# Performance work log

Hardware: AMD Instinct MI355X
Metric: run time of the kernel (lower is better)

Reference implementation:

```python
import jax, jax.numpy as jnp
import numpy as np

B = 8
A = 1614
TOPN = 6
IOU_THR = 0.25
PAD = 224
OUT = 224

def _make_anchors():
    # 6 anchor shapes on the 14x14 map, 6 on 7x7, 9 on 4x4 -> 1614 total,
    # ordered anchor-type-major then row-major spatial to match the [C,H,W] flatten
    # of the tidy conv outputs (as generate_default_anchor_maps does in NTS-Net).
    specs = [
        (14, 32.0, [(48, 48), (64, 48), (48, 64), (80, 80), (96, 64), (64, 96)]),
        (7, 64.0, [(96, 96), (128, 96), (96, 128), (160, 160), (192, 128), (128, 192)]),
        (4, 112.0, [(192, 192), (256, 192), (192, 256), (288, 288), (320, 256), (256, 320), (352, 352), (384, 320), (320, 384)]),
    ]
    blocks = []
    for fm, stride, sizes in specs:
        c = (np.arange(fm) + 0.5) * stride
        cy, cx = np.meshgrid(c, c, indexing='ij')
        for (h, w) in sizes:
            blocks.append(np.stack([cy - h / 2, cx - w / 2, cy + h / 2, cx + w / 2], -1).reshape(-1, 4))
    a = (np.concatenate(blocks, 0) + PAD).astype(np.int64)  # mimic (edge_anchors+224).astype(int)
    return a.astype(np.float32)  # [1614,4] (y0,x0,y1,x1) in padded-image coords

def _conv(x, w, b, stride, pad):
    y = jax.lax.conv_general_dilated(x, w, (stride, stride), [(pad, pad), (pad, pad)],
                                     dimension_numbers=('NCHW', 'OIHW', 'NCHW'))
    return y + b[None, :, None, None]

def _rpn_scores(rpn, wd1, bd1, wd2, bd2, wd3, bd3, wt1, bt1, wt2, bt2, wt3, bt3):
    b = rpn.shape[0]
    d1 = jax.nn.relu(_conv(rpn, wd1, bd1, 1, 1))   # [B,128,14,14]
    d2 = jax.nn.relu(_conv(d1, wd2, bd2, 2, 1))    # [B,128,7,7]
    d3 = jax.nn.relu(_conv(d2, wd3, bd3, 2, 1))    # [B,128,4,4]
    t1 = _conv(d1, wt1, bt1, 1, 0).reshape(b, -1)  # [B,1176]
    t2 = _conv(d2, wt2, bt2, 1, 0).reshape(b, -1)  # [B,294]
    t3 = _conv(d3, wt3, bt3, 1, 0).reshape(b, -1)  # [B,144]
    return jnp.concatenate([t1, t2, t3], axis=1)   # [B,1614]

def _nms_keep(boxes, scores):
    # Greedy NMS over all A anchors; returns keep mask in ORIGINAL anchor order.
    order = jnp.argsort(-scores)
    b = boxes[order]
    y0, x0, y1, x1 = b[:, 0], b[:, 1], b[:, 2], b[:, 3]
    area = (y1 - y0) * (x1 - x0)
    ih = jnp.clip(jnp.minimum(y1[:, None], y1[None, :]) - jnp.maximum(y0[:, None], y0[None, :]), 0)
    iw = jnp.clip(jnp.minimum(x1[:, None], x1[None, :]) - jnp.maximum(x0[:, None], x0[None, :]), 0)
    inter = ih * iw
    iou = inter / (area[:, None] + area[None, :] - inter)
    idx = jnp.arange(A)
    def body(i, supp):
        row = (iou[i] > IOU_THR) & (idx > i)
        return jnp.where(supp[i], supp, supp | row)
    supp = jax.lax.fori_loop(0, A, body, jnp.zeros((A,), bool))
    return jnp.zeros((A,), bool).at[order].set(~supp)

def _crop_resize(img, box):
    # img [3,Hp,Wp]; box int32 (x0,y0,x1,y1).
    # Equivalent to F.interpolate(img[:, y0:y1, x0:x1], (224,224), 'bilinear', align_corners=True)
    x0, y0, x1, y1 = box[0], box[1], box[2], box[3]
    t = jnp.arange(OUT, dtype=jnp.float32) / (OUT - 1)
    sy = y0.astype(jnp.float32) + t * (y1 - 1 - y0).astype(jnp.float32)
    sx = x0.astype(jnp.float32) + t * (x1 - 1 - x0).astype(jnp.float32)
    y0i = jnp.floor(sy).astype(jnp.int32); x0i = jnp.floor(sx).astype(jnp.int32)
    y1i = jnp.minimum(y0i + 1, y1 - 1);    x1i = jnp.minimum(x0i + 1, x1 - 1)
    wy = (sy - y0i.astype(jnp.float32))[None, :, None]
    wx = (sx - x0i.astype(jnp.float32))[None, None, :]
    g = lambda yi, xi: img[:, yi][:, :, xi]  # gather rows then cols -> [3,224,224]
    top = (1 - wx) * g(y0i, x0i) + wx * g(y0i, x1i)
    bot = (1 - wx) * g(y1i, x0i) + wx * g(y1i, x1i)
    return (1 - wy) * top + wy * bot

def setup_inputs():
    key = jax.random.key(0)
    ks = jax.random.split(key, 16)
    n = jax.random.normal
    return {
        'x': n(ks[0], (B, 3, 448, 448), jnp.float32),
        'rpn_feature': n(ks[1], (B, 2048, 14, 14), jnp.float32),
        'anchors': jnp.asarray(_make_anchors()),
        'wd1': 0.02 * n(ks[2], (128, 2048, 3, 3), jnp.float32), 'bd1': 0.01 * n(ks[3], (128,), jnp.float32),
        'wd2': 0.05 * n(ks[4], (128, 128, 3, 3), jnp.float32),  'bd2': 0.01 * n(ks[5], (128,), jnp.float32),
        'wd3': 0.05 * n(ks[6], (128, 128, 3, 3), jnp.float32),  'bd3': 0.01 * n(ks[7], (128,), jnp.float32),
        'wt1': 0.1 * n(ks[8], (6, 128, 1, 1), jnp.float32),     'bt1': 0.01 * n(ks[9], (6,), jnp.float32),
        'wt2': 0.1 * n(ks[10], (6, 128, 1, 1), jnp.float32),    'bt2': 0.01 * n(ks[11], (6,), jnp.float32),
        'wt3': 0.1 * n(ks[12], (9, 128, 1, 1), jnp.float32),    'bt3': 0.01 * n(ks[13], (9,), jnp.float32),
    }

def reference(x, rpn_feature, anchors, wd1, bd1, wd2, bd2, wd3, bd3, wt1, bt1, wt2, bt2, wt3, bt3):
    scores = _rpn_scores(rpn_feature, wd1, bd1, wd2, bd2, wd3, bd3, wt1, bt1, wt2, bt2, wt3, bt3)
    keep = jax.vmap(lambda s: _nms_keep(anchors, s))(scores)           # [B,A] bool
    masked = jnp.where(keep, scores, -jnp.inf)
    top_prob, top_idx = jax.lax.top_k(masked, TOPN)                    # [B,6]
    tb = anchors[top_idx]                                              # [B,6,4] (y0,x0,y1,x1)
    coords = jnp.stack([tb[..., 1], tb[..., 0], tb[..., 3], tb[..., 2]], -1)  # (x0,y0,x1,y1)
    x_pad = jnp.pad(x, ((0, 0), (0, 0), (PAD, PAD), (PAD, PAD)))       # [B,3,896,896]
    bint = coords.astype(jnp.int32)
    part_imgs = jax.vmap(lambda img, bs: jax.vmap(lambda bb: _crop_resize(img, bb))(bs))(x_pad, bint)  # [B,6,3,224,224]
    return part_imgs, coords, top_prob, top_idx
```

## Files before the change

### kernel.cpp

```cpp
#include <hip/hip_runtime.h>
#include <hip/hip_bf16.h>
#include <math.h>
#include <stdint.h>


#define OFF_COORDS 7225344
#define OFF_PROB   7225536
#define OFF_IDX    7225584
#define NA 1614
#define K1TOT 18432

typedef __attribute__((ext_vector_type(8)))  short  short8;
typedef __attribute__((ext_vector_type(16))) float  floatx16;

__device__ inline void split_bf16(float v, unsigned short& h, unsigned short& l)
{
    __hip_bfloat16 hb = __float2bfloat16(v);
    float hv = __bfloat162float(hb);
    __hip_bfloat16 lb = __float2bfloat16(v - hv);
    h = *reinterpret_cast<unsigned short*>(&hb);
    l = *reinterpret_cast<unsigned short*>(&lb);
}

__global__ __launch_bounds__(256) void k_prep(const float* __restrict__ rpn,
                                              const float* __restrict__ w1,
                                              const float* __restrict__ w2,
                                              const float* __restrict__ w3,
                                              unsigned short* __restrict__ ah,
                                              unsigned short* __restrict__ al,
                                              unsigned short* __restrict__ b1h,
                                              unsigned short* __restrict__ b1l,
                                              unsigned short* __restrict__ b2h,
                                              unsigned short* __restrict__ b2l,
                                              unsigned short* __restrict__ b3h,
                                              unsigned short* __restrict__ b3l)
{
    __shared__ float tileA[64][65];
    __shared__ float tileB[9][260];
    const int bid = blockIdx.x;
    const int t   = threadIdx.x;

    if (bid < 1024) {
        const int cib  = (bid & 31) * 64;
        const int posb = ((bid >> 5) & 3) * 64;
        const int b    = bid >> 7;
#pragma unroll
        for (int it = 0; it < 16; ++it) {
            int idx  = it * 256 + t;
            int cil  = idx >> 6;
            int posl = idx & 63;
            int pos  = posb + posl;
            int py = pos >> 4, px = pos & 15;
            int y = py - 1, x = px - 1;
            float v = 0.0f;
            if ((unsigned)y < 14u && (unsigned)x < 14u)
                v = rpn[((size_t)(b * 2048 + cib + cil) * 14 + y) * 14 + x];
            tileA[cil][posl] = v;
        }
        __syncthreads();
#pragma unroll
        for (int it = 0; it < 16; ++it) {
            int idx  = it * 256 + t;
            int posl = idx >> 6;
            int cil  = idx & 63;
            float v = tileA[cil][posl];
            unsigned short h, l;
            split_bf16(v, h, l);
            size_t o = (size_t)(b * 256 + posb + posl) * 2048 + cib + cil;
            ah[o] = h; al[o] = l;
        }
    } else if (bid < 2048) {
        const int lb  = bid - 1024;
        const int ci0 = (lb & 7) * 256;
        const int co  = lb >> 3;
        const float* wc = w1 + (size_t)co * K1TOT + (size_t)ci0 * 9;
#pragma unroll
        for (int it = 0; it < 9; ++it) {
            int i = it * 256 + t;
            float v = wc[i];
            tileB[i % 9][i / 9] = v;
        }
        __syncthreads();
#pragma unroll
        for (int tap = 0; tap < 9; ++tap) {
            float v = tileB[tap][t];
            unsigned short h, l;
            split_bf16(v, h, l);
            size_t o = (size_t)co * K1TOT + (size_t)tap * 2048 + ci0 + t;
            b1h[o] = h; b1l[o] = l;
        }
    } else {
        const int lb  = bid - 2048;
        const int tap = lb % 9;
        const int co  = lb / 9;
        const int z   = t >> 7;
        const int ci  = t & 127;
        const float* w = z ? w3 : w2;
        unsigned short* bh = z ? b3h : b2h;
        unsigned short* bl = z ? b3l : b2l;
        float v = w[((size_t)co * 128 + ci) * 9 + tap];
        unsigned short h, l;
        split_bf16(v, h, l);
        size_t o = (size_t)co * 1152 + tap * 128 + ci;
        bh[o] = h; bl[o] = l;
    }
}

template<int POSN, int OW, int STR, int CIN, int MTOT>
__global__ __launch_bounds__(256) void k_conv_mfma(const short* __restrict__ ah,
                                                   const short* __restrict__ al,
                                                   const short* __restrict__ bh,
                                                   const short* __restrict__ bl,
                                                   float* __restrict__ partial,
                                                   int chunk)
{
    constexpr int KTOT = CIN * 9;
    __shared__ short AsH[128][40];
    __shared__ short AsL[128][40];
    __shared__ short BsH[128][40];
    __shared__ short BsL[128][40];

    const int t     = threadIdx.x;
    const int lane  = t & 63;
    const int w     = t >> 6;
    const int wm    = (w & 1) * 64;
    const int wn    = (w >> 1) * 64;
    const int lm    = lane & 31;
    const int half  = lane >> 5;
    const int mbase = blockIdx.x * 128;
    const int k0    = blockIdx.y * chunk;
    const int k1    = (k0 + chunk < KTOT) ? (k0 + chunk) : KTOT;

    int arow[2], apos[2]; bool aval[2];
    const int akc = (t & 3) * 8;
#pragma unroll
    for (int i = 0; i < 2; ++i) {
        int row = ((i * 256 + t) >> 2);
        int m   = mbase + row;
        arow[i] = row;
        aval[i] = (m < MTOT);
        int mm = aval[i] ? m : 0;
        int b  = mm / POSN;
        int p  = mm - b * POSN;
        int y  = p / OW;
        int x  = p - y * OW;
        apos[i] = b * 256 + y * STR * 16 + x * STR;
    }

    floatx16 acc[2][2];
#pragma unroll
    for (int mf = 0; mf < 2; ++mf)
#pragma unroll
        for (int nf = 0; nf < 2; ++nf)
#pragma unroll
            for (int r = 0; r < 16; ++r) acc[mf][nf][r] = 0.0f;

    const short8 zero8 = {0, 0, 0, 0, 0, 0, 0, 0};

    for (int ks = k0; ks < k1; ks += 32) {
        const int tap = ks / CIN;
        const int ci0 = ks - tap * CIN;
        const int dy  = tap / 3, dx = tap - dy * 3;
#pragma unroll
        for (int i = 0; i < 2; ++i) {
            short8 vh = zero8, vl = zero8;
            if (aval[i]) {
                size_t g = (size_t)(apos[i] + dy * 16 + dx) * CIN + ci0 + akc;
                vh = *(const short8*)(ah + g);
                vl = *(const short8*)(al + g);
            }
            *(short8*)&AsH[arow[i]][akc] = vh;
            *(short8*)&AsL[arow[i]][akc] = vl;
        }
#pragma unroll
        for (int i = 0; i < 2; ++i) {
            int n = ((i * 256 + t) >> 2);
            size_t g = (size_t)n * KTOT + ks + akc;
            *(short8*)&BsH[n][akc] = *(const short8*)(bh + g);
            *(short8*)&BsL[n][akc] = *(const short8*)(bl + g);
        }
        __syncthreads();
#pragma unroll
        for (int kst = 0; kst < 2; ++kst) {
            const int koff = kst * 16 + half * 8;
            short8 a_h[2], a_l[2], b_h[2], b_l[2];
#pragma unroll
            for (int mf = 0; mf < 2; ++mf) {
                a_h[mf] = *(const short8*)&AsH[wm + mf * 32 + lm][koff];
                a_l[mf] = *(const short8*)&AsL[wm + mf * 32 + lm][koff];
            }
#pragma unroll
            for (int nf = 0; nf < 2; ++nf) {
                b_h[nf] = *(const short8*)&BsH[wn + nf * 32 + lm][koff];
                b_l[nf] = *(const short8*)&BsL[wn + nf * 32 + lm][koff];
            }
#pragma unroll
            for (int mf = 0; mf < 2; ++mf)
#pragma unroll
                for (int nf = 0; nf < 2; ++nf) {
                    acc[mf][nf] = __builtin_amdgcn_mfma_f32_32x32x16_bf16(
                        a_h[mf], b_h[nf], acc[mf][nf], 0, 0, 0);
                    acc[mf][nf] = __builtin_amdgcn_mfma_f32_32x32x16_bf16(
                        a_h[mf], b_l[nf], acc[mf][nf], 0, 0, 0);
                    acc[mf][nf] = __builtin_amdgcn_mfma_f32_32x32x16_bf16(
                        a_l[mf], b_h[nf], acc[mf][nf], 0, 0, 0);
                }
        }
        __syncthreads();
    }

    float* P = partial + (size_t)blockIdx.y * MTOT * 128;
#pragma unroll
    for (int mf = 0; mf < 2; ++mf)
#pragma unroll
        for (int nf = 0; nf < 2; ++nf)
#pragma unroll
            for (int r = 0; r < 16; ++r) {
                int row = (r & 3) + 8 * (r >> 2) + 4 * half;
                int m = mbase + wm + mf * 32 + row;
                int n = wn + nf * 32 + lm;
                if (m < MTOT) P[(size_t)m * 128 + n] = acc[mf][nf][r];
            }
}

template<int POSN, int OW, int STR, int CIN, int MTOT>
__global__ __launch_bounds__(128) void k_conv64(const short* __restrict__ ah,
                                                const short* __restrict__ al,
                                                const short* __restrict__ bh,
                                                const short* __restrict__ bl,
                                                float* __restrict__ partial,
                                                int chunk)
{
    constexpr int KTOT = CIN * 9;
    __shared__ short AsH[64][40];
    __shared__ short AsL[64][40];
    __shared__ short BsH[128][40];
    __shared__ short BsL[128][40];

    const int t     = threadIdx.x;
    const int lane  = t & 63;
    const int w     = t >> 6;
    const int wn    = w * 64;
    const int lm    = lane & 31;
    const int half  = lane >> 5;
    const int mbase = blockIdx.x * 64;
    const int kc    = blockIdx.y;
    const int k0    = kc * chunk;
    const int k1    = (k0 + chunk < KTOT) ? (k0 + chunk) : KTOT;

    const int akc = (t & 3) * 8;
    int arow[2], apos[2]; bool aval[2];
#pragma unroll
    for (int i = 0; i < 2; ++i) {
        int slot = i * 128 + t;
        int row  = slot >> 2;
        int m    = mbase + row;
        arow[i] = row;
        aval[i] = (m < MTOT);
        int mm = aval[i] ? m : 0;
        int b  = mm / POSN;
        int p  = mm - b * POSN;
        int y  = p / OW;
        int x  = p - y * OW;
        apos[i] = b * 256 + y * STR * 16 + x * STR;
    }

    floatx16 acc[2][2];
#pragma unroll
    for (int mf = 0; mf < 2; ++mf)
#pragma unroll
        for (int nf = 0; nf < 2; ++nf)
#pragma unroll
            for (int r = 0; r < 16; ++r) acc[mf][nf][r] = 0.0f;

    const short8 zero8 = {0, 0, 0, 0, 0, 0, 0, 0};

    for (int ks = k0; ks < k1; ks += 32) {
        const int tap = ks / CIN;
        const int ci0 = ks - tap * CIN;
        const int dy  = tap / 3, dx = tap - dy * 3;
#pragma unroll
        for (int i = 0; i < 2; ++i) {
            short8 vh = zero8, vl = zero8;
            if (aval[i]) {
                size_t g = (size_t)(apos[i] + dy * 16 + dx) * CIN + ci0 + akc;
                vh = *(const short8*)(ah + g);
                vl = *(const short8*)(al + g);
            }
            *(short8*)&AsH[arow[i]][akc] = vh;
            *(short8*)&AsL[arow[i]][akc] = vl;
        }
#pragma unroll
        for (int j = 0; j < 4; ++j) {
            int n = ((j * 128 + t) >> 2);
            size_t g = (size_t)n * KTOT + ks + akc;
            *(short8*)&BsH[n][akc] = *(const short8*)(bh + g);
            *(short8*)&BsL[n][akc] = *(const short8*)(bl + g);
        }
        __syncthreads();
#pragma unroll
        for (int kst = 0; kst < 2; ++kst) {
            const int koff = kst * 16 + half * 8;
            short8 a_h[2], a_l[2], b_h[2], b_l[2];
#pragma unroll
            for (int mf = 0; mf < 2; ++mf) {
                a_h[mf] = *(const short8*)&AsH[mf * 32 + lm][koff];
                a_l[mf] = *(const short8*)&AsL[mf * 32 + lm][koff];
            }
#pragma unroll
            for (int nf = 0; nf < 2; ++nf) {
                b_h[nf] = *(const short8*)&BsH[wn + nf * 32 + lm][koff];
                b_l[nf] = *(const short8*)&BsL[wn + nf * 32 + lm][koff];
            }
#pragma unroll
            for (int mf = 0; mf < 2; ++mf)
#pragma unroll
                for (int nf = 0; nf < 2; ++nf) {
                    acc[mf][nf] = __builtin_amdgcn_mfma_f32_32x32x16_bf16(
                        a_h[mf], b_h[nf], acc[mf][nf], 0, 0, 0);
                    acc[mf][nf] = __builtin_amdgcn_mfma_f32_32x32x16_bf16(
                        a_h[mf], b_l[nf], acc[mf][nf], 0, 0, 0);
                    acc[mf][nf] = __builtin_amdgcn_mfma_f32_32x32x16_bf16(
                        a_l[mf], b_h[nf], acc[mf][nf], 0, 0, 0);
                }
        }
        __syncthreads();
    }

    float* P = partial + (size_t)kc * MTOT * 128;
#pragma unroll
    for (int mf = 0; mf < 2; ++mf)
#pragma unroll
        for (int nf = 0; nf < 2; ++nf)
#pragma unroll
            for (int r = 0; r < 16; ++r) {
                int row = (r & 3) + 8 * (r >> 2) + 4 * half;
                int m = mbase + mf * 32 + row;
                int n = wn + nf * 32 + lm;
                if (m < MTOT) P[(size_t)m * 128 + n] = acc[mf][nf][r];
            }
}

template<int POSN, int OWV>
__global__ __launch_bounds__(256) void k_reduce_pad(const float* __restrict__ partial,
                                                    const float* __restrict__ bias,
                                                    float* __restrict__ dn,
                                                    __hip_bfloat16* __restrict__ ph,
                                                    __hip_bfloat16* __restrict__ pl,
                                                    int S)
{
    constexpr int MTOT = 8 * POSN;
    int idx = blockIdx.x * 256 + threadIdx.x;
    int b   = idx >> 13;
    int pos = (idx >> 5) & 255;
    int c4  = idx & 31;
    int y = (pos >> 4) - 1;
    int x = (pos & 15) - 1;
    if ((unsigned)y < (unsigned)OWV && (unsigned)x < (unsigned)OWV) {
        int m = b * POSN + y * OWV + x;
        float4 s = ((const float4*)bias)[c4];
        for (int k = 0; k < S; ++k) {
            float4 p = ((const float4*)(partial + (size_t)k * MTOT * 128 + (size_t)m * 128))[c4];
            s.x += p.x; s.y += p.y; s.z += p.z; s.w += p.w;
        }
        s.x = fmaxf(s.x, 0.0f); s.y = fmaxf(s.y, 0.0f);
        s.z = fmaxf(s.z, 0.0f); s.w = fmaxf(s.w, 0.0f);
        ((float4*)dn)[(size_t)m * 32 + c4] = s;
        ushort4 h, l;
        split_bf16(s.x, h.x, l.x);
        split_bf16(s.y, h.y, l.y);
        split_bf16(s.z, h.z, l.z);
        split_bf16(s.w, h.w, l.w);
        ((ushort4*)ph)[idx] = h;
        ((ushort4*)pl)[idx] = l;
    } else {
        ushort4 z = {0, 0, 0, 0};
        ((ushort4*)ph)[idx] = z;
        ((ushort4*)pl)[idx] = z;
    }
}

__global__ __launch_bounds__(256) void k_reduce3(const float* __restrict__ partial,
                                                 const float* __restrict__ bias,
                                                 float* __restrict__ dn, int S)
{
    int idx = blockIdx.x * 256 + threadIdx.x;
    int c4  = idx & 31;
    float4 s = ((const float4*)bias)[c4];
    for (int k = 0; k < S; ++k) {
        float4 p = ((const float4*)(partial + (size_t)k * 128 * 128))[idx];
        s.x += p.x; s.y += p.y; s.z += p.z; s.w += p.w;
    }
    s.x = fmaxf(s.x, 0.0f); s.y = fmaxf(s.y, 0.0f);
    s.z = fmaxf(s.z, 0.0f); s.w = fmaxf(s.w, 0.0f);
    ((float4*)dn)[idx] = s;
}

__global__ __launch_bounds__(256) void k_heads(const float* __restrict__ d1n,
                                               const float* __restrict__ d2n,
                                               const float* __restrict__ d3n,
                                               const float* __restrict__ w1, const float* __restrict__ b1,
                                               const float* __restrict__ w2, const float* __restrict__ b2,
                                               const float* __restrict__ w3, const float* __restrict__ b3,
                                               float* __restrict__ scores)
{
    int idx = blockIdx.x * 256 + threadIdx.x;
    if (idx >= 8 * NA) return;
    int b = idx / NA;
    int e = idx - b * NA;
    const float* d; const float* w; float bias;
    if (e < 1176) {
        int c = e / 196, p = e - c * 196;
        d = d1n + (size_t)(b * 196 + p) * 128; w = w1 + c * 128; bias = b1[c];
    } else if (e < 1470) {
        int e2 = e - 1176; int c = e2 / 49, p = e2 - c * 49;
        d = d2n + (size_t)(b * 49 + p) * 128; w = w2 + c * 128; bias = b2[c];
    } else {
        int e2 = e - 1470; int c = e2 / 16, p = e2 - c * 16;
        d = d3n + (size_t)(b * 16 + p) * 128; w = w3 + c * 128; bias = b3[c];
    }
    float s = bias;
#pragma unroll
    for (int i = 0; i < 32; ++i) {
        float4 dv = ((const float4*)d)[i];
        float4 wv = ((const float4*)w)[i];
        s = fmaf(dv.x, wv.x, s);
        s = fmaf(dv.y, wv.y, s);
        s = fmaf(dv.z, wv.z, s);
        s = fmaf(dv.w, wv.w, s);
    }
    scores[idx] = s;
}

__global__ __launch_bounds__(256) void k_nms_topk(const float* __restrict__ scores,
                                                  const float* __restrict__ anchors,
                                                  float* __restrict__ out,
                                                  int* __restrict__ boxes)
{
    __shared__ float ms[NA];
    __shared__ float ay0[NA], ax0[NA], ay1[NA], ax1[NA];
    __shared__ unsigned char picked[NA];
    __shared__ float rv[4]; __shared__ int ri[4];
    __shared__ float win[5];
    int b = blockIdx.x;
    int t = threadIdx.x;
    for (int i = t; i < NA; i += 256) {
        ms[i] = scores[b * NA + i];
        float4 an = ((const float4*)anchors)[i];
        ay0[i] = an.x; ax0[i] = an.y; ay1[i] = an.z; ax1[i] = an.w;
        picked[i] = 0;
    }
    __syncthreads();
    for (int r = 0; r < 6; ++r) {
        float bv = -INFINITY; int bi = NA;
        for (int i = t; i < NA; i += 256) {
            if (!picked[i]) {
                float v = ms[i];
                if (v > bv || (v == bv && i < bi)) { bv = v; bi = i; }
            }
        }
#pragma unroll
        for (int off = 32; off > 0; off >>= 1) {
            float v2 = __shfl_down(bv, off);
            int   i2 = __shfl_down(bi, off);
            if (v2 > bv || (v2 == bv && i2 < bi)) { bv = v2; bi = i2; }
        }
        if ((t & 63) == 0) { rv[t >> 6] = bv; ri[t >> 6] = bi; }
        __syncthreads();
        if (t == 0) {
            bv = rv[0]; bi = ri[0];
            for (int wv = 1; wv < 4; ++wv)
                if (rv[wv] > bv || (rv[wv] == bv && ri[wv] < bi)) { bv = rv[wv]; bi = ri[wv]; }
            picked[bi] = 1;
            win[0] = ay0[bi]; win[1] = ax0[bi]; win[2] = ay1[bi]; win[3] = ax1[bi]; win[4] = bv;
            int o = b * 6 + r;
            out[OFF_COORDS + o * 4 + 0] = ax0[bi];
            out[OFF_COORDS + o * 4 + 1] = ay0[bi];
            out[OFF_COORDS + o * 4 + 2] = ax1[bi];
            out[OFF_COORDS + o * 4 + 3] = ay1[bi];
            out[OFF_PROB + o] = bv;
            out[OFF_IDX  + o] = (float)bi;
            boxes[o * 4 + 0] = (int)ax0[bi];
            boxes[o * 4 + 1] = (int)ay0[bi];
            boxes[o * 4 + 2] = (int)ax1[bi];
            boxes[o * 4 + 3] = (int)ay1[bi];
        }
        __syncthreads();
        float by0 = win[0], bx0 = win[1], by1 = win[2], bx1 = win[3];
        float barea = (by1 - by0) * (bx1 - bx0);
        for (int i = t; i < NA; i += 256) {
            if (picked[i]) continue;
            float ih = fmaxf(fminf(by1, ay1[i]) - fmaxf(by0, ay0[i]), 0.0f);
            float iw = fmaxf(fminf(bx1, ax1[i]) - fmaxf(bx0, ax0[i]), 0.0f);
            float inter = ih * iw;
            float area  = (ay1[i] - ay0[i]) * (ax1[i] - ax0[i]);
            float iou = inter / (barea + area - inter);
            if (iou > 0.25f) ms[i] = -INFINITY;
        }
        __syncthreads();
    }
}

__global__ __launch_bounds__(256) void k_crop4(const float* __restrict__ x,
                                               const int* __restrict__ boxes,
                                               float* __restrict__ out)
{
    int idx = blockIdx.x * 256 + threadIdx.x;
    int qi  = idx % 56;
    int j   = (idx / 56) % 224;
    int rem = idx / (56 * 224);
    int c   = rem % 3;
    int br  = rem / 3;
    int b   = br / 6;
    int4 bx = ((const int4*)boxes)[br];
    float tj = (float)j / 223.0f;
    float sy = (float)bx.y + tj * (float)(bx.w - 1 - bx.y);
    int y0i = (int)floorf(sy);
    int y1i = min(y0i + 1, bx.w - 1);
    float wy = sy - (float)y0i;
    const float* img = x + ((size_t)b * 3 + c) * 448 * 448;
    auto g = [&](int yy, int xx) -> float {
        yy -= 224; xx -= 224;
        if ((unsigned)yy >= 448u || (unsigned)xx >= 448u) return 0.0f;
        return img[(size_t)yy * 448 + xx];
    };
    float4 o;
#pragma unroll
    for (int e = 0; e < 4; ++e) {
        int i = qi * 4 + e;
        float ti = (float)i / 223.0f;
        float sx = (float)bx.x + ti * (float)(bx.z - 1 - bx.x);
        int x0i = (int)floorf(sx);
        int x1i = min(x0i + 1, bx.z - 1);
        float wx = sx - (float)x0i;
        float g00 = g(y0i, x0i), g01 = g(y0i, x1i);
        float g10 = g(y1i, x0i), g11 = g(y1i, x1i);
        float top = (1.0f - wx) * g00 + wx * g01;
        float bot = (1.0f - wx) * g10 + wx * g11;
        float v = (1.0f - wy) * top + wy * bot;
        if (e == 0) o.x = v; else if (e == 1) o.y = v;
        else if (e == 2) o.z = v; else o.w = v;
    }
    ((float4*)out)[idx] = o;
}

extern "C" void kernel_launch(void* const* d_in, const int* in_sizes, int n_in,
                              void* d_out, int out_size, void* d_ws, size_t ws_size,
                              hipStream_t stream)
{
    (void)in_sizes; (void)n_in; (void)out_size;
    const float* x    = (const float*)d_in[0];
    const float* rpn  = (const float*)d_in[1];
    const float* anch = (const float*)d_in[2];
    const float* wd1  = (const float*)d_in[3];
    const float* bd1  = (const float*)d_in[4];
    const float* wd2  = (const float*)d_in[5];
    const float* bd2  = (const float*)d_in[6];
    const float* wd3  = (const float*)d_in[7];
    const float* bd3  = (const float*)d_in[8];
    const float* hw1  = (const float*)d_in[9];
    const float* hb1  = (const float*)d_in[10];
    const float* hw2  = (const float*)d_in[11];
    const float* hb2  = (const float*)d_in[12];
    const float* hw3  = (const float*)d_in[13];
    const float* hb3  = (const float*)d_in[14];
    float* out = (float*)d_out;

    char* ws = (char*)d_ws;
    size_t off = 0;
    auto alloc = [&](size_t bytes) -> void* {
        void* p = ws + off;
        off = (off + bytes + 255) & ~(size_t)255;
        return p;
    };
    unsigned short* ahb = (unsigned short*)alloc((size_t)8 * 256 * 2048 * 2);
    unsigned short* alb = (unsigned short*)alloc((size_t)8 * 256 * 2048 * 2);
    unsigned short* b1h = (unsigned short*)alloc((size_t)128 * K1TOT * 2);
    unsigned short* b1l = (unsigned short*)alloc((size_t)128 * K1TOT * 2);
    unsigned short* b2h = (unsigned short*)alloc((size_t)128 * 1152 * 2);
    unsigned short* b2l = (unsigned short*)alloc((size_t)128 * 1152 * 2);
    unsigned short* b3h = (unsigned short*)alloc((size_t)128 * 1152 * 2);
    unsigned short* b3l = (unsigned short*)alloc((size_t)128 * 1152 * 2);
    __hip_bfloat16* d1ph = (__hip_bfloat16*)alloc((size_t)8 * 256 * 128 * 2);
    __hip_bfloat16* d1pl = (__hip_bfloat16*)alloc((size_t)8 * 256 * 128 * 2);
    __hip_bfloat16* d2ph = (__hip_bfloat16*)alloc((size_t)8 * 256 * 128 * 2);
    __hip_bfloat16* d2pl = (__hip_bfloat16*)alloc((size_t)8 * 256 * 128 * 2);
    float* d1n  = (float*)alloc((size_t)8 * 196 * 128 * 4);
    float* d2n  = (float*)alloc((size_t)8 * 49 * 128 * 4);
    float* d3n  = (float*)alloc((size_t)8 * 16 * 128 * 4);
    float* sc   = (float*)alloc((size_t)8 * NA * 4);
    int*  boxes = (int*)alloc((size_t)8 * 6 * 4 * 4);
    size_t avail = (ws_size > off) ? (ws_size - off) : 0;
    float* P = (float*)(ws + off);

    long long s1 = (long long)(avail / ((size_t)1568 * 128 * 4));
    if (s1 > 48) s1 = 48;
    if (s1 < 1)  s1 = 1;
    int S1 = (int)s1;
    int chunk1 = ((K1TOT + S1 * 32 - 1) / (S1 * 32)) * 32;

    k_prep<<<dim3(3200), 256, 0, stream>>>(rpn, wd1, wd2, wd3,
        ahb, alb, b1h, b1l, b2h, b2l, b3h, b3l);

    k_conv_mfma<196, 14, 1, 2048, 1568><<<dim3(13, S1), 256, 0, stream>>>(
        (const short*)ahb, (const short*)alb, (const short*)b1h, (const short*)b1l, P, chunk1);
    k_reduce_pad<196, 14><<<dim3(256), 256, 0, stream>>>(P, bd1, d1n, d1ph, d1pl, S1);

    k_conv64<49, 7, 2, 128, 392><<<dim3(7, 36), 128, 0, stream>>>(
        (const short*)d1ph, (const short*)d1pl, (const short*)b2h, (const short*)b2l, P, 32);
    k_reduce_pad<49, 7><<<dim3(256), 256, 0, stream>>>(P, bd2, d2n, d2ph, d2pl, 36);

    k_conv64<16, 4, 2, 128, 128><<<dim3(2, 36), 128, 0, stream>>>(
        (const short*)d2ph, (const short*)d2pl, (const short*)b3h, (const short*)b3l, P, 32);
    k_reduce3<<<dim3(16), 256, 0, stream>>>(P, bd3, d3n, 36);

    k_heads<<<dim3((8 * NA + 255) / 256), 256, 0, stream>>>(d1n, d2n, d3n,
        hw1, hb1, hw2, hb2, hw3, hb3, sc);

    k_nms_topk<<<dim3(8), 256, 0, stream>>>(sc, anch, out, boxes);

    k_crop4<<<dim3(7056), 256, 0, stream>>>(x, boxes, out);
}
```

Measured before the change: 253.7 us.

## Fuse post-conv1 pipeline into one cooperative persistent kernel with grid syncs

```diff
diff --git a/kernel.cpp b/kernel.cpp
--- a/kernel.cpp
+++ b/kernel.cpp
@@ -1,7 +1,10 @@
 #include <hip/hip_runtime.h>
 #include <hip/hip_bf16.h>
+#include <hip/hip_cooperative_groups.h>
 #include <math.h>
 #include <stdint.h>
+
+namespace cg = cooperative_groups;
 
 
 #define OFF_COORDS 7225344
@@ -107,18 +110,18 @@
 }
 
 template<int POSN, int OW, int STR, int CIN, int MTOT>
-__global__ __launch_bounds__(256) void k_conv_mfma(const short* __restrict__ ah,
-                                                   const short* __restrict__ al,
-                                                   const short* __restrict__ bh,
-                                                   const short* __restrict__ bl,
-                                                   float* __restrict__ partial,
-                                                   int chunk)
+__device__ void conv_tile(const short* __restrict__ ah,
+                          const short* __restrict__ al,
+                          const short* __restrict__ bh,
+                          const short* __restrict__ bl,
+                          float* __restrict__ partial,
+                          int mb, int kc, int chunk, char* smem)
 {
     constexpr int KTOT = CIN * 9;
-    __shared__ short AsH[128][40];
-    __shared__ short AsL[128][40];
-    __shared__ short BsH[128][40];
-    __shared__ short BsL[128][40];
+    short (*AsH)[40] = (short(*)[40])(smem);
+    short (*AsL)[40] = (short(*)[40])(smem + 10240);
+    short (*BsH)[40] = (short(*)[40])(smem + 20480);
+    short (*BsL)[40] = (short(*)[40])(smem + 30720);
 
     const int t     = threadIdx.x;
     const int lane  = t & 63;
@@ -127,8 +130,8 @@
     const int wn    = (w >> 1) * 64;
     const int lm    = lane & 31;
     const int half  = lane >> 5;
-    const int mbase = blockIdx.x * 128;
-    const int k0    = blockIdx.y * chunk;
+    const int mbase = mb * 128;
+    const int k0    = kc * chunk;
     const int k1    = (k0 + chunk < KTOT) ? (k0 + chunk) : KTOT;
 
     int arow[2], apos[2]; bool aval[2];
@@ -209,7 +212,7 @@
         __syncthreads();
     }
 
-    float* P = partial + (size_t)blockIdx.y * MTOT * 128;
+    float* P = partial + (size_t)kc * MTOT * 128;
 #pragma unroll
     for (int mf = 0; mf < 2; ++mf)
 #pragma unroll
@@ -223,134 +226,14 @@
             }
 }
 
-template<int POSN, int OW, int STR, int CIN, int MTOT>
-__global__ __launch_bounds__(128) void k_conv64(const short* __restrict__ ah,
-                                                const short* __restrict__ al,
-                                                const short* __restrict__ bh,
-                                                const short* __restrict__ bl,
-                                                float* __restrict__ partial,
-                                                int chunk)
-{
-    constexpr int KTOT = CIN * 9;
-    __shared__ short AsH[64][40];
-    __shared__ short AsL[64][40];
-    __shared__ short BsH[128][40];
-    __shared__ short BsL[128][40];
-
-    const int t     = threadIdx.x;
-    const int lane  = t & 63;
-    const int w     = t >> 6;
-    const int wn    = w * 64;
-    const int lm    = lane & 31;
-    const int half  = lane >> 5;
-    const int mbase = blockIdx.x * 64;
-    const int kc    = blockIdx.y;
-    const int k0    = kc * chunk;
-    const int k1    = (k0 + chunk < KTOT) ? (k0 + chunk) : KTOT;
-
-    const int akc = (t & 3) * 8;
-    int arow[2], apos[2]; bool aval[2];
-#pragma unroll
-    for (int i = 0; i < 2; ++i) {
-        int slot = i * 128 + t;
-        int row  = slot >> 2;
-        int m    = mbase + row;
-        arow[i] = row;
-        aval[i] = (m < MTOT);
-        int mm = aval[i] ? m : 0;
-        int b  = mm / POSN;
-        int p  = mm - b * POSN;
-        int y  = p / OW;
-        int x  = p - y * OW;
-        apos[i] = b * 256 + y * STR * 16 + x * STR;
-    }
-
-    floatx16 acc[2][2];
-#pragma unroll
-    for (int mf = 0; mf < 2; ++mf)
-#pragma unroll
-        for (int nf = 0; nf < 2; ++nf)
-#pragma unroll
-            for (int r = 0; r < 16; ++r) acc[mf][nf][r] = 0.0f;
-
-    const short8 zero8 = {0, 0, 0, 0, 0, 0, 0, 0};
-
-    for (int ks = k0; ks < k1; ks += 32) {
-        const int tap = ks / CIN;
-        const int ci0 = ks - tap * CIN;
-        const int dy  = tap / 3, dx = tap - dy * 3;
-#pragma unroll
-        for (int i = 0; i < 2; ++i) {
-            short8 vh = zero8, vl = zero8;
-            if (aval[i]) {
-                size_t g = (size_t)(apos[i] + dy * 16 + dx) * CIN + ci0 + akc;
-                vh = *(const short8*)(ah + g);
-                vl = *(const short8*)(al + g);
-            }
-            *(short8*)&AsH[arow[i]][akc] = vh;
-            *(short8*)&AsL[arow[i]][akc] = vl;
-        }
-#pragma unroll
-        for (int j = 0; j < 4; ++j) {
-            int n = ((j * 128 + t) >> 2);
-            size_t g = (size_t)n * KTOT + ks + akc;
-            *(short8*)&BsH[n][akc] = *(const short8*)(bh + g);
-            *(short8*)&BsL[n][akc] = *(const short8*)(bl + g);
-        }
-        __syncthreads();
-#pragma unroll
-        for (int kst = 0; kst < 2; ++kst) {
-            const int koff = kst * 16 + half * 8;
-            short8 a_h[2], a_l[2], b_h[2], b_l[2];
-#pragma unroll
-            for (int mf = 0; mf < 2; ++mf) {
-                a_h[mf] = *(const short8*)&AsH[mf * 32 + lm][koff];
-                a_l[mf] = *(const short8*)&AsL[mf * 32 + lm][koff];
-            }
-#pragma unroll
-            for (int nf = 0; nf < 2; ++nf) {
-                b_h[nf] = *(const short8*)&BsH[wn + nf * 32 + lm][koff];
-                b_l[nf] = *(const short8*)&BsL[wn + nf * 32 + lm][koff];
-            }
-#pragma unroll
-            for (int mf = 0; mf < 2; ++mf)
-#pragma unroll
-                for (int nf = 0; nf < 2; ++nf) {
-                    acc[mf][nf] = __builtin_amdgcn_mfma_f32_32x32x16_bf16(
-                        a_h[mf], b_h[nf], acc[mf][nf], 0, 0, 0);
-                    acc[mf][nf] = __builtin_amdgcn_mfma_f32_32x32x16_bf16(
-                        a_h[mf], b_l[nf], acc[mf][nf], 0, 0, 0);
-                    acc[mf][nf] = __builtin_amdgcn_mfma_f32_32x32x16_bf16(
-                        a_l[mf], b_h[nf], acc[mf][nf], 0, 0, 0);
-                }
-        }
-        __syncthreads();
-    }
-
-    float* P = partial + (size_t)kc * MTOT * 128;
-#pragma unroll
-    for (int mf = 0; mf < 2; ++mf)
-#pragma unroll
-        for (int nf = 0; nf < 2; ++nf)
-#pragma unroll
-            for (int r = 0; r < 16; ++r) {
-                int row = (r & 3) + 8 * (r >> 2) + 4 * half;
-                int m = mbase + mf * 32 + row;
-                int n = wn + nf * 32 + lm;
-                if (m < MTOT) P[(size_t)m * 128 + n] = acc[mf][nf][r];
-            }
-}
-
 template<int POSN, int OWV>
-__global__ __launch_bounds__(256) void k_reduce_pad(const float* __restrict__ partial,
-                                                    const float* __restrict__ bias,
-                                                    float* __restrict__ dn,
-                                                    __hip_bfloat16* __restrict__ ph,
-                                                    __hip_bfloat16* __restrict__ pl,
-                                                    int S)
+__device__ void reduce_pad_slot(int idx, const float* __restrict__ partial,
+                                const float* __restrict__ bias,
+                                float* __restrict__ dn,
+                                __hip_bfloat16* __restrict__ ph,
+                                __hip_bfloat16* __restrict__ pl, int S)
 {
     constexpr int MTOT = 8 * POSN;
-    int idx = blockIdx.x * 256 + threadIdx.x;
     int b   = idx >> 13;
     int pos = (idx >> 5) & 255;
     int c4  = idx & 31;
@@ -380,12 +263,11 @@
     }
 }
 
-__global__ __launch_bounds__(256) void k_reduce3(const float* __restrict__ partial,
-                                                 const float* __restrict__ bias,
-                                                 float* __restrict__ dn, int S)
-{
-    int idx = blockIdx.x * 256 + threadIdx.x;
-    int c4  = idx & 31;
+__device__ void reduce3_slot(int idx, const float* __restrict__ partial,
+                             const float* __restrict__ bias,
+                             float* __restrict__ dn, int S)
+{
+    int c4 = idx & 31;
     float4 s = ((const float4*)bias)[c4];
     for (int k = 0; k < S; ++k) {
         float4 p = ((const float4*)(partial + (size_t)k * 128 * 128))[idx];
@@ -396,15 +278,15 @@
     ((float4*)dn)[idx] = s;
 }
 
-__global__ __launch_bounds__(256) void k_heads(const float* __restrict__ d1n,
-                                               const float* __restrict__ d2n,
-                                               const float* __restrict__ d3n,
-                                               const float* __restrict__ w1, const float* __restrict__ b1,
-                                               const float* __restrict__ w2, const float* __restrict__ b2,
-                                               const float* __restrict__ w3, const float* __restrict__ b3,
-                                               float* __restrict__ scores)
-{
-    int idx = blockIdx.x * 256 + threadIdx.x;
+__device__ void heads_one(int idx,
+                          const float* __restrict__ d1n,
+                          const float* __restrict__ d2n,
+                          const float* __restrict__ d3n,
+                          const float* __restrict__ w1, const float* __restrict__ b1,
+                          const float* __restrict__ w2, const float* __restrict__ b2,
+                          const float* __restrict__ w3, const float* __restrict__ b3,
+                          float* __restrict__ scores)
+{
     if (idx >= 8 * NA) return;
     int b = idx / NA;
     int e = idx - b * NA;
@@ -432,17 +314,21 @@
     scores[idx] = s;
 }
 
-__global__ __launch_bounds__(256) void k_nms_topk(const float* __restrict__ scores,
-                                                  const float* __restrict__ anchors,
-                                                  float* __restrict__ out,
-                                                  int* __restrict__ boxes)
-{
-    __shared__ float ms[NA];
-    __shared__ float ay0[NA], ax0[NA], ay1[NA], ax1[NA];
-    __shared__ unsigned char picked[NA];
-    __shared__ float rv[4]; __shared__ int ri[4];
-    __shared__ float win[5];
-    int b = blockIdx.x;
+__device__ void nms_block(int b, char* smem,
+                          const float* __restrict__ scores,
+                          const float* __restrict__ anchors,
+                          float* __restrict__ out,
+                          int* __restrict__ boxes)
+{
+    float* ms  = (float*)smem;
+    float* ay0 = ms + NA;
+    float* ax0 = ay0 + NA;
+    float* ay1 = ax0 + NA;
+    float* ax1 = ay1 + NA;
+    unsigned char* picked = (unsigned char*)(ax1 + NA);
+    float* rv  = (float*)(picked + ((NA + 15) & ~15));
+    int*   ri  = (int*)(rv + 4);
+    float* win = (float*)(ri + 4);
     int t = threadIdx.x;
     for (int i = t; i < NA; i += 256) {
         ms[i] = scores[b * NA + i];
@@ -472,7 +358,7 @@
             for (int wv = 1; wv < 4; ++wv)
                 if (rv[wv] > bv || (rv[wv] == bv && ri[wv] < bi)) { bv = rv[wv]; bi = ri[wv]; }
             picked[bi] = 1;
-            win[0] = ay0[bi]; win[1] = ax0[bi]; win[2] = ay1[bi]; win[3] = ax1[bi]; win[4] = bv;
+            win[0] = ay0[bi]; win[1] = ax0[bi]; win[2] = ay1[bi]; win[3] = ax1[bi];
             int o = b * 6 + r;
             out[OFF_COORDS + o * 4 + 0] = ax0[bi];
             out[OFF_COORDS + o * 4 + 1] = ay0[bi];
@@ -501,11 +387,10 @@
     }
 }
 
-__global__ __launch_bounds__(256) void k_crop4(const float* __restrict__ x,
-                                               const int* __restrict__ boxes,
-                                               float* __restrict__ out)
-{
-    int idx = blockIdx.x * 256 + threadIdx.x;
+__device__ void crop4_one(int idx, const float* __restrict__ x,
+                          const int* __restrict__ boxes,
+                          float* __restrict__ out)
+{
     int qi  = idx % 56;
     int j   = (idx / 56) % 224;
     int rem = idx / (56 * 224);
@@ -542,6 +427,114 @@
         else if (e == 2) o.z = v; else o.w = v;
     }
     ((float4*)out)[idx] = o;
+}
+
+template<int POSN, int OW, int STR, int CIN, int MTOT>
+__global__ __launch_bounds__(256) void k_conv_mfma(const short* __restrict__ ah,
+                                                   const short* __restrict__ al,
+                                                   const short* __restrict__ bh,
+                                                   const short* __restrict__ bl,
+                                                   float* __restrict__ partial,
+                                                   int chunk)
+{
+    __shared__ short8 smemv[2560];
+    conv_tile<POSN, OW, STR, CIN, MTOT>(ah, al, bh, bl, partial,
+                                        blockIdx.x, blockIdx.y, chunk, (char*)smemv);
+}
+
+template<int POSN, int OWV>
+__global__ __launch_bounds__(256) void k_reduce_pad(const float* __restrict__ partial,
+                                                    const float* __restrict__ bias,
+                                                    float* __restrict__ dn,
+                                                    __hip_bfloat16* __restrict__ ph,
+                                                    __hip_bfloat16* __restrict__ pl,
+                                                    int S)
+{
+    reduce_pad_slot<POSN, OWV>(blockIdx.x * 256 + threadIdx.x, partial, bias, dn, ph, pl, S);
+}
+
+__global__ __launch_bounds__(256) void k_reduce3(const float* __restrict__ partial,
+                                                 const float* __restrict__ bias,
+                                                 float* __restrict__ dn, int S)
+{
+    reduce3_slot(blockIdx.x * 256 + threadIdx.x, partial, bias, dn, S);
+}
+
+__global__ __launch_bounds__(256) void k_heads(const float* __restrict__ d1n,
+                                               const float* __restrict__ d2n,
+                                               const float* __restrict__ d3n,
+                                               const float* __restrict__ w1, const float* __restrict__ b1,
+                                               const float* __restrict__ w2, const float* __restrict__ b2,
+                                               const float* __restrict__ w3, const float* __restrict__ b3,
+                                               float* __restrict__ scores)
+{
+    heads_one(blockIdx.x * 256 + threadIdx.x, d1n, d2n, d3n, w1, b1, w2, b2, w3, b3, scores);
+}
+
+__global__ __launch_bounds__(256) void k_nms_topk(const float* __restrict__ scores,
+                                                  const float* __restrict__ anchors,
+                                                  float* __restrict__ out,
+                                                  int* __restrict__ boxes)
+{
+    __shared__ short8 smemv[2560];
+    nms_block(blockIdx.x, (char*)smemv, scores, anchors, out, boxes);
+}
+
+__global__ __launch_bounds__(256) void k_crop4(const float* __restrict__ x,
+                                               const int* __restrict__ boxes,
+                                               float* __restrict__ out)
+{
+    crop4_one(blockIdx.x * 256 + threadIdx.x, x, boxes, out);
+}
+
+struct TailArgs {
+    float *P1, *P2, *P3;
+    const float *bd1, *bd2, *bd3;
+    float *d1n, *d2n, *d3n;
+    __hip_bfloat16 *d1ph, *d1pl, *d2ph, *d2pl;
+    const short *b2h, *b2l, *b3h, *b3l;
+    const float *hw1, *hb1, *hw2, *hb2, *hw3, *hb3;
+    float *sc;
+    const float *anch;
+    float *out;
+    int *boxes;
+    const float *x;
+    int S1;
+};
+
+__global__ __launch_bounds__(256, 4) void k_megatail(TailArgs a)
+{
+    __shared__ short8 smemv[2560];
+    char* smem = (char*)smemv;
+    cg::grid_group grid = cg::this_grid();
+    const int t = threadIdx.x;
+    const int gs = gridDim.x * 256;
+
+    for (int idx = blockIdx.x * 256 + t; idx < 8 * 256 * 32; idx += gs)
+        reduce_pad_slot<196, 14>(idx, a.P1, a.bd1, a.d1n, a.d1ph, a.d1pl, a.S1);
+    grid.sync();
+    for (int vb = blockIdx.x; vb < 144; vb += gridDim.x)
+        conv_tile<49, 7, 2, 128, 392>((const short*)a.d1ph, (const short*)a.d1pl,
+                                      a.b2h, a.b2l, a.P2, vb & 3, vb >> 2, 32, smem);
+    grid.sync();
+    for (int idx = blockIdx.x * 256 + t; idx < 8 * 256 * 32; idx += gs)
+        reduce_pad_slot<49, 7>(idx, a.P2, a.bd2, a.d2n, a.d2ph, a.d2pl, 36);
+    grid.sync();
+    for (int vb = blockIdx.x; vb < 36; vb += gridDim.x)
+        conv_tile<16, 4, 2, 128, 128>((const short*)a.d2ph, (const short*)a.d2pl,
+                                      a.b3h, a.b3l, a.P3, 0, vb, 32, smem);
+    grid.sync();
+    for (int idx = blockIdx.x * 256 + t; idx < 4096; idx += gs)
+        reduce3_slot(idx, a.P3, a.bd3, a.d3n, 36);
+    grid.sync();
+    for (int idx = blockIdx.x * 256 + t; idx < 8 * NA; idx += gs)
+        heads_one(idx, a.d1n, a.d2n, a.d3n, a.hw1, a.hb1, a.hw2, a.hb2, a.hw3, a.hb3, a.sc);
+    grid.sync();
+    for (int vb = blockIdx.x; vb < 8; vb += gridDim.x)
+        nms_block(vb, smem, a.sc, a.anch, a.out, a.boxes);
+    grid.sync();
+    for (int idx = blockIdx.x * 256 + t; idx < 48 * 3 * 224 * 56; idx += gs)
+        crop4_one(idx, a.x, a.boxes, a.out);
 }
 
 extern "C" void kernel_launch(void* const* d_in, const int* in_sizes, int n_in,
@@ -590,8 +583,10 @@
     float* d3n  = (float*)alloc((size_t)8 * 16 * 128 * 4);
     float* sc   = (float*)alloc((size_t)8 * NA * 4);
     int*  boxes = (int*)alloc((size_t)8 * 6 * 4 * 4);
+    float* P2   = (float*)alloc((size_t)36 * 392 * 128 * 4);
+    float* P3   = (float*)alloc((size_t)36 * 128 * 128 * 4);
     size_t avail = (ws_size > off) ? (ws_size - off) : 0;
-    float* P = (float*)(ws + off);
+    float* P1 = (float*)(ws + off);
 
     long long s1 = (long long)(avail / ((size_t)1568 * 128 * 4));
     if (s1 > 48) s1 = 48;
@@ -603,21 +598,56 @@
         ahb, alb, b1h, b1l, b2h, b2l, b3h, b3l);
 
     k_conv_mfma<196, 14, 1, 2048, 1568><<<dim3(13, S1), 256, 0, stream>>>(
-        (const short*)ahb, (const short*)alb, (const short*)b1h, (const short*)b1l, P, chunk1);
-    k_reduce_pad<196, 14><<<dim3(256), 256, 0, stream>>>(P, bd1, d1n, d1ph, d1pl, S1);
-
-    k_conv64<49, 7, 2, 128, 392><<<dim3(7, 36), 128, 0, stream>>>(
-        (const short*)d1ph, (const short*)d1pl, (const short*)b2h, (const short*)b2l, P, 32);
-    k_reduce_pad<49, 7><<<dim3(256), 256, 0, stream>>>(P, bd2, d2n, d2ph, d2pl, 36);
-
-    k_conv64<16, 4, 2, 128, 128><<<dim3(2, 36), 128, 0, stream>>>(
-        (const short*)d2ph, (const short*)d2pl, (const short*)b3h, (const short*)b3l, P, 32);
-    k_reduce3<<<dim3(16), 256, 0, stream>>>(P, bd3, d3n, 36);
-
-    k_heads<<<dim3((8 * NA + 255) / 256), 256, 0, stream>>>(d1n, d2n, d3n,
-        hw1, hb1, hw2, hb2, hw3, hb3, sc);
-
-    k_nms_topk<<<dim3(8), 256, 0, stream>>>(sc, anch, out, boxes);
-
-    k_crop4<<<dim3(7056), 256, 0, stream>>>(x, boxes, out);
-}
+        (const short*)ahb, (const short*)alb, (const short*)b1h, (const short*)b1l, P1, chunk1);
+
+    static int coopBlocks = -1;
+    if (coopBlocks < 0) {
+        int maxB = 0;
+        hipError_t e = hipOccupancyMaxActiveBlocksPerMultiprocessor(
+            &maxB, reinterpret_cast<const void*>(k_megatail), 256, 0);
+        if (e == hipSuccess && maxB > 0) {
+            int nCU = 256;
+            hipDeviceProp_t prop;
+            if (hipGetDeviceProperties(&prop, 0) == hipSuccess && prop.multiProcessorCount > 0)
+                nCU = prop.multiProcessorCount;
+            if (maxB > 4) maxB = 4;
+            coopBlocks = maxB * nCU;
+        } else {
+            coopBlocks = 0;
+        }
+    }
+
+    bool legacy = true;
+    if (coopBlocks >= 256) {
+        TailArgs ta;
+        ta.P1 = P1; ta.P2 = P2; ta.P3 = P3;
+        ta.bd1 = bd1; ta.bd2 = bd2; ta.bd3 = bd3;
+        ta.d1n = d1n; ta.d2n = d2n; ta.d3n = d3n;
+        ta.d1ph = d1ph; ta.d1pl = d1pl; ta.d2ph = d2ph; ta.d2pl = d2pl;
+        ta.b2h = (const short*)b2h; ta.b2l = (const short*)b2l;
+        ta.b3h = (const short*)b3h; ta.b3l = (const short*)b3l;
+        ta.hw1 = hw1; ta.hb1 = hb1; ta.hw2 = hw2; ta.hb2 = hb2; ta.hw3 = hw3; ta.hb3 = hb3;
+        ta.sc = sc; ta.anch = anch; ta.out = out; ta.boxes = boxes; ta.x = x;
+        ta.S1 = S1;
+        void* args[] = { &ta };
+        hipError_t e = hipLaunchCooperativeKernel(
+            reinterpret_cast<const void*>(k_megatail),
+            dim3(coopBlocks), dim3(256), args, 0, stream);
+        if (e == hipSuccess) legacy = false;
+        else coopBlocks = 0;
+    }
+
+    if (legacy) {
+        k_reduce_pad<196, 14><<<dim3(256), 256, 0, stream>>>(P1, bd1, d1n, d1ph, d1pl, S1);
+        k_conv_mfma<49, 7, 2, 128, 392><<<dim3(4, 36), 256, 0, stream>>>(
+            (const short*)d1ph, (const short*)d1pl, (const short*)b2h, (const short*)b2l, P2, 32);
+        k_reduce_pad<49, 7><<<dim3(256), 256, 0, stream>>>(P2, bd2, d2n, d2ph, d2pl, 36);
+        k_conv_mfma<16, 4, 2, 128, 128><<<dim3(1, 36), 256, 0, stream>>>(
+            (const short*)d2ph, (const short*)d2pl, (const short*)b3h, (const short*)b3l, P3, 32);
+        k_reduce3<<<dim3(16), 256, 0, stream>>>(P3, bd3, d3n, 36);
+        k_heads<<<dim3((8 * NA + 255) / 256), 256, 0, stream>>>(d1n, d2n, d3n,
+            hw1, hb1, hw2, hb2, hw3, hb3, sc);
+        k_nms_topk<<<dim3(8), 256, 0, stream>>>(sc, anch, out, boxes);
+        k_crop4<<<dim3(7056), 256, 0, stream>>>(x, boxes, out);
+    }
+}
```

After: 260.7 us. 1.03x slower.
